# Kernel tuning notes

Hardware: AMD Instinct MI355X
Metric: run time of the kernel (lower is better)

Reference implementation:

```python
import jax, jax.numpy as jnp
import numpy as np
import math

XLEN, YLEN, B = 2048, 1024, 8
XD, YD, HD, YOUT = 1024, 1024, 512, 1024


def setup_inputs() -> dict:
    key = jax.random.key(0)
    ks = jax.random.split(key, 12)

    def lin(kw, kb, out_d, in_d):
        s = 1.0 / math.sqrt(in_d)
        w = jax.random.uniform(kw, (out_d, in_d), jnp.float32, -s, s)
        b = jax.random.uniform(kb, (out_d,), jnp.float32, -s, s)
        return w, b

    Xk_w, Xk_b = lin(ks[0], ks[1], HD, XD)
    Xv_w, Xv_b = lin(ks[2], ks[3], HD, XD)
    Yq_w, Yq_b = lin(ks[4], ks[5], HD, YD)
    Yw_w, Yw_b = lin(ks[6], ks[7], YOUT, YD + HD)

    X = jax.random.normal(ks[8], (XLEN, B, XD), jnp.float32)
    Y = jax.random.normal(ks[9], (YLEN, B, YD), jnp.float32)
    alignment = jax.random.normal(ks[10], (B, YLEN, XLEN), jnp.float32)
    X_pad_mask = jax.random.bernoulli(ks[11], 0.1, (B, YLEN, XLEN))  # True -> mask out
    align_w = jnp.zeros((1,), jnp.float32)  # nn.Parameter([0])

    return {"X": X, "Y": Y, "alignment": alignment, "X_pad_mask": X_pad_mask,
            "Xk_w": Xk_w, "Xk_b": Xk_b, "Xv_w": Xv_w, "Xv_b": Xv_b,
            "Yq_w": Yq_w, "Yq_b": Yq_b, "Yw_w": Yw_w, "Yw_b": Yw_b,
            "align_w": align_w}


def reference(X, Y, alignment, X_pad_mask, Xk_w, Xk_b, Xv_w, Xv_b,
              Yq_w, Yq_b, Yw_w, Yw_b, align_w):
    FMAX = jnp.finfo(X.dtype).max
    # projections (torch Linear: x @ W.T + b)
    xk = X @ Xk_w.T + Xk_b                     # (x, b, hd)
    yq = Y @ Yq_w.T + Yq_b                     # (y, b, hd)
    # scaled cross-attention logits
    logit = jnp.einsum('xbd,ybd->byx', xk, yq) / math.sqrt(xk.shape[-1])
    # gated alignment bias + clamp
    logit = logit + jax.nn.sigmoid(align_w[0]) * alignment
    logit = jnp.maximum(logit, -FMAX)
    # pad-mask additive fill (-FMAX) then clamp (matches masked_fill + add + clamp)
    logit = jnp.maximum(logit + jnp.where(X_pad_mask, -FMAX, 0.0), -FMAX)
    attn = jax.nn.softmax(logit, axis=-1)      # (b, y, x); dropout = identity (eval)
    xv = X @ Xv_w.T + Xv_b                     # (x, b, hd)
    attn_feat = jnp.einsum('byx,xbh->ybh', attn, xv)  # (y, b, hd)
    concat = jnp.concatenate([Y, attn_feat], axis=-1)  # (y, b, yd+hd)
    return concat @ Yw_w.T + Yw_b              # (y, b, y_outdim)
```

## Files before the change

### kernel.cpp

```cpp
#include <hip/hip_runtime.h>


#define FMAXF 3.402823466e38f

typedef __attribute__((ext_vector_type(8))) __bf16 bf16x8;
typedef __attribute__((ext_vector_type(4))) float f32x4;

static __device__ __forceinline__ short f2b(float f) {
  union { float f; unsigned u; } x; x.f = f;
  unsigned r = (x.u + 0x7FFFu + ((x.u >> 16) & 1u)) >> 16;
  return (short)r;
}
static __device__ __forceinline__ float b2f(short s) {
  union { unsigned u; float f; } x; x.u = ((unsigned)(unsigned short)s) << 16;
  return x.f;
}

static __device__ __forceinline__ void gl_lds16(const short* g, short* l) {
  __builtin_amdgcn_global_load_lds(
      (const __attribute__((address_space(1))) void*)g,
      (__attribute__((address_space(3))) void*)l, 16, 0, 0);
}


struct EpiKV {
  static constexpr bool staged = true;
  static constexpr bool expm = false;
  static constexpr bool norm = false;
  short* xk; short* xv; const float* kb; const float* vb;
  __device__ float bias_at(int n) const { return n < 512 ? kb[n] : vb[n - 512]; }
  __device__ void store(int bz, int m, int n, int4 v) const {
    int b = m & 7; long x = m >> 3;
    if (n < 512) *(int4*)(xk + ((long)b * 2048 + x) * 512 + n) = v;
    else         *(int4*)(xv + ((long)b * 2048 + x) * 512 + (n - 512)) = v;
  }
};

struct EpiYq {
  static constexpr bool staged = true;
  static constexpr bool expm = false;
  static constexpr bool norm = false;
  short* out; const float* bias;
  __device__ float bias_at(int n) const { return bias[n]; }
  __device__ void store(int bz, int m, int n, int4 v) const {
    *(int4*)(out + (((long)(m & 7)) * 1024 + (m >> 3)) * 512 + n) = v;
  }
};

struct EpiLogitExp {
  static constexpr bool staged = true;
  static constexpr bool expm = true;
  static constexpr bool norm = false;
  short* out;
  const float* align;
  const int* mask;
  const float* alw;
  float* rowsum;
  __device__ float bias_at(int n) const { return 0.0f; }
  __device__ void store(int bz, int m, int n, int4 v) const {
    *(int4*)(out + ((long)bz * 1024 + m) * 2048 + n) = v;
  }
};

struct EpiConcatNorm {
  static constexpr bool staged = true;
  static constexpr bool expm = false;
  static constexpr bool norm = true;
  short* out; const float* rowsum;
  __device__ float bias_at(int n) const { return 0.0f; }
  __device__ void store(int bz, int m, int n, int4 v) const {
    *(int4*)(out + ((long)m * 8 + bz) * 1536 + 1024 + n) = v;
  }
};

struct EpiOut {
  static constexpr bool staged = false;
  static constexpr bool expm = false;
  static constexpr bool norm = false;
  float* out; const float* bias;
  __device__ void direct(int bz, int m, int n, float v) const {
    out[(long)m * 1024 + n] = v + bias[n];
  }
};

template <int TM, typename Epi>
__global__ __launch_bounds__(256) void gemm_mt(
    const short* __restrict__ A, long sAb, int lda,
    const short* __restrict__ B, long sBb, int ldb,
    int K, int tlog, Epi epi) {
  constexpr int R = TM + 128;
  constexpr int SEGS = R / 32;
  constexpr int LDSN = (R * 64 > TM * 128) ? R * 64 : TM * 128;
  __shared__ short S[LDSN];

  const int tid = threadIdx.x;
  const int lane = tid & 63, wave = tid >> 6;
  const int bz = blockIdx.z;

  const int id = blockIdx.x;
  const int xcd = id & 7;
  const int rr = id >> 3;
  const int n0 = (rr & ((1 << tlog) - 1)) * 128;
  const int m0 = (((rr >> tlog) << 3) + xcd) * TM;

  const short* gp[SEGS];
#pragma unroll
  for (int t = 0; t < SEGS; t++) {
    int slot = t * 256 + tid;
    int row = slot >> 3;
    int gcol = ((slot & 7) ^ (row & 7)) * 8;
    gp[t] = (row < TM)
                ? A + (long)bz * sAb + (long)(m0 + row) * lda + gcol
                : B + (long)bz * sBb + (long)(n0 + row - TM) * ldb + gcol;
  }

  const int wm = (TM == 128) ? (wave & 1) * 64 : 0;
  const int wn = (TM == 128) ? (wave >> 1) * 64 : wave * 32;
  constexpr int MI = 4;
  constexpr int MJ = (TM == 128) ? 4 : 2;
  const int quad = lane >> 4, l16 = lane & 15;
  const int xr = l16 & 7;

  f32x4 acc[MI][MJ] = {};

  for (int k0 = 0; k0 < K; k0 += 64) {
#pragma unroll
    for (int t = 0; t < SEGS; t++)
      gl_lds16(gp[t] + k0, S + (t * 256 + tid) * 8);
    __syncthreads();

#pragma unroll
    for (int kk = 0; kk < 2; kk++) {
      union { int4 v; bf16x8 f; } a[MI], b[MJ];
      const int g = ((kk << 2) + quad);
#pragma unroll
      for (int i = 0; i < MI; i++)
        a[i].v = *(const int4*)(S + (wm + i * 16 + l16) * 64 + (g ^ xr) * 8);
#pragma unroll
      for (int j = 0; j < MJ; j++)
        b[j].v = *(const int4*)(S + (TM + wn + j * 16 + l16) * 64 + (g ^ xr) * 8);
#pragma unroll
      for (int i = 0; i < MI; i++)
#pragma unroll
        for (int j = 0; j < MJ; j++)
          acc[i][j] = __builtin_amdgcn_mfma_f32_16x16x32_bf16(a[i].f, b[j].f,
                                                              acc[i][j], 0, 0, 0);
    }
    __syncthreads();
  }

  if constexpr (Epi::staged) {
    if constexpr (Epi::norm) {
#pragma unroll
      for (int i = 0; i < MI; i++)
#pragma unroll
        for (int r = 0; r < 4; r++) {
          const int row = wm + i * 16 + quad * 4 + r;
          const float inv = 1.0f / epi.rowsum[(long)bz * 1024 + m0 + row];
#pragma unroll
          for (int j = 0; j < MJ; j++)
            S[row * 128 + wn + j * 16 + l16] = f2b(acc[i][j][r] * inv);
        }
    } else {
#pragma unroll
      for (int j = 0; j < MJ; j++) {
        const int c = wn + j * 16 + l16;
        const float bj = epi.bias_at(n0 + c);
#pragma unroll
        for (int i = 0; i < MI; i++)
#pragma unroll
          for (int r = 0; r < 4; r++)
            S[(wm + i * 16 + quad * 4 + r) * 128 + c] = f2b(acc[i][j][r] + bj);
      }
    }
    __syncthreads();

    if constexpr (Epi::expm) {
      const float g = 1.0f / (1.0f + __expf(-epi.alw[0]));
      const float scale = 0.04419417382415922f;
#pragma unroll
      for (int t = 0; t < TM / 16; t++) {
        const int c = t * 256 + tid;
        const int row = c >> 4, colc = (c & 15) * 8;
        const long gy = (long)bz * 1024 + m0 + row;
        const float* ap = epi.align + gy * 2048 + n0 + colc;
        const int*   mp = epi.mask + gy * 2048 + n0 + colc;
        float4 a0 = *(const float4*)ap;
        float4 a1 = *(const float4*)(ap + 4);
        int4 q0 = *(const int4*)mp;
        int4 q1 = *(const int4*)(mp + 4);
        union { short s[8]; int4 v; } d;
        d.v = *(const int4*)(S + row * 128 + colc);
        float e[8];
        e[0] = q0.x ? 0.0f : __expf(fmaf(b2f(d.s[0]), scale, g * a0.x));
        e[1] = q0.y ? 0.0f : __expf(fmaf(b2f(d.s[1]), scale, g * a0.y));
        e[2] = q0.z ? 0.0f : __expf(fmaf(b2f(d.s[2]), scale, g * a0.z));
        e[3] = q0.w ? 0.0f : __expf(fmaf(b2f(d.s[3]), scale, g * a0.w));
        e[4] = q1.x ? 0.0f : __expf(fmaf(b2f(d.s[4]), scale, g * a1.x));
        e[5] = q1.y ? 0.0f : __expf(fmaf(b2f(d.s[5]), scale, g * a1.y));
        e[6] = q1.z ? 0.0f : __expf(fmaf(b2f(d.s[6]), scale, g * a1.z));
        e[7] = q1.w ? 0.0f : __expf(fmaf(b2f(d.s[7]), scale, g * a1.w));
        float part = 0.0f;
#pragma unroll
        for (int k = 0; k < 8; k++) { part += e[k]; d.s[k] = f2b(e[k]); }
        epi.store(bz, m0 + row, n0 + colc, d.v);
        part += __shfl_xor(part, 1);
        part += __shfl_xor(part, 2);
        part += __shfl_xor(part, 4);
        part += __shfl_xor(part, 8);
        if ((tid & 15) == 0) atomicAdd(epi.rowsum + gy, part);
      }
    } else {
#pragma unroll
      for (int t = 0; t < TM / 16; t++) {
        int c = t * 256 + tid;
        int row = c >> 4, colc = (c & 15) * 8;
        int4 v = *(const int4*)(S + row * 128 + colc);
        epi.store(bz, m0 + row, n0 + colc, v);
      }
    }
  } else {
#pragma unroll
    for (int i = 0; i < MI; i++)
#pragma unroll
      for (int j = 0; j < MJ; j++)
#pragma unroll
        for (int r = 0; r < 4; r++)
          epi.direct(bz, m0 + wm + i * 16 + quad * 4 + r,
                     n0 + wn + j * 16 + l16, acc[i][j][r]);
  }
}

__global__ __launch_bounds__(256) void cvt_f32_bf16(const float* __restrict__ in,
                                                    short* __restrict__ out,
                                                    long n4) {
  long i = (long)blockIdx.x * 256 + threadIdx.x;
  if (i >= n4) return;
  float4 f = ((const float4*)in)[i];
  union { short s[4]; long long v; } o;
  o.s[0] = f2b(f.x); o.s[1] = f2b(f.y); o.s[2] = f2b(f.z); o.s[3] = f2b(f.w);
  ((long long*)out)[i] = o.v;
}

__global__ __launch_bounds__(256) void cvt_weights(
    const float* __restrict__ xk_w, const float* __restrict__ xv_w,
    const float* __restrict__ yq_w, const float* __restrict__ yw_w,
    short* __restrict__ wkv, short* __restrict__ wyq, short* __restrict__ wyw,
    float* __restrict__ rowsum) {
  long i = (long)blockIdx.x * 256 + threadIdx.x;
  if (i < 8192) rowsum[i] = 0.0f;
  const float* src; long long* dst; long off;
  if (i < 131072)      { src = xk_w; dst = (long long*)wkv; off = i; }
  else if (i < 262144) { src = xv_w; dst = (long long*)wkv + 131072; off = i - 131072; }
  else if (i < 393216) { src = yq_w; dst = (long long*)wyq; off = i - 262144; }
  else                 { src = yw_w; dst = (long long*)wyw; off = i - 393216; }
  float4 f = ((const float4*)src)[off];
  union { short s[4]; long long v; } o;
  o.s[0] = f2b(f.x); o.s[1] = f2b(f.y); o.s[2] = f2b(f.z); o.s[3] = f2b(f.w);
  dst[off] = o.v;
}

__global__ __launch_bounds__(256) void cvt_y_concat(const float* __restrict__ in,
                                                    short* __restrict__ out) {
  long idx = (long)blockIdx.x * 256 + threadIdx.x;
  long row = idx >> 8;
  int c = (int)(idx & 255) << 2;
  float4 f = *(const float4*)(in + row * 1024 + c);
  union { short s[4]; unsigned long long v; } o;
  o.s[0] = f2b(f.x); o.s[1] = f2b(f.y); o.s[2] = f2b(f.z); o.s[3] = f2b(f.w);
  *(unsigned long long*)(out + row * 1536 + c) = o.v;
}

__global__ __launch_bounds__(256) void transpose_xv(const short* __restrict__ xv,
                                                    short* __restrict__ xvt) {
  __shared__ short t[32][36];
  const int b = blockIdx.z;
  const long x0 = (long)blockIdx.x * 32, h0 = (long)blockIdx.y * 32;
  const int r = threadIdx.x >> 3, c = (threadIdx.x & 7) * 4;
  const short* src = xv + ((long)b * 2048 + x0 + r) * 512 + h0 + c;
  *(int2*)&t[r][c] = *(const int2*)src;
  __syncthreads();
  union { short s[4]; int2 v; } o;
  o.s[0] = t[c + 0][r]; o.s[1] = t[c + 1][r];
  o.s[2] = t[c + 2][r]; o.s[3] = t[c + 3][r];
  short* dst = xvt + ((long)b * 512 + h0 + r) * 2048 + x0 + c;
  *(int2*)dst = o.v;
}


extern "C" void kernel_launch(void* const* d_in, const int* in_sizes, int n_in,
                              void* d_out, int out_size, void* d_ws, size_t ws_size,
                              hipStream_t stream) {
  const float* X    = (const float*)d_in[0];
  const float* Y    = (const float*)d_in[1];
  const float* alig = (const float*)d_in[2];
  const int*   mask = (const int*)d_in[3];
  const float* Xk_w = (const float*)d_in[4];
  const float* Xk_b = (const float*)d_in[5];
  const float* Xv_w = (const float*)d_in[6];
  const float* Xv_b = (const float*)d_in[7];
  const float* Yq_w = (const float*)d_in[8];
  const float* Yq_b = (const float*)d_in[9];
  const float* Yw_w = (const float*)d_in[10];
  const float* Yw_b = (const float*)d_in[11];
  const float* alw  = (const float*)d_in[12];
  float* out = (float*)d_out;

  char* ws = (char*)d_ws;
  short* xbf    = (short*)(ws + 0);
  short* E      = (short*)(ws + 0);
  short* xk     = (short*)(ws + 33554432);
  short* xv     = (short*)(ws + 50331648);
  short* xvt    = (short*)(ws + 67108864);
  short* yq     = (short*)(ws + 83886080);
  short* concat = (short*)(ws + 92274688);
  short* wkv    = (short*)(ws + 117440512);
  short* wyq    = (short*)(ws + 119537664);
  short* wyw    = (short*)(ws + 120586240);
  float* rowsum = (float*)(ws + 123731968);

  cvt_f32_bf16<<<16384, 256, 0, stream>>>(X, xbf, 4194304);
  cvt_y_concat<<<8192, 256, 0, stream>>>(Y, concat);
  cvt_weights<<<3072, 256, 0, stream>>>(Xk_w, Xv_w, Yq_w, Yw_w, wkv, wyq, wyw,
                                        rowsum);

  gemm_mt<128, EpiKV><<<dim3(1024, 1, 1), 256, 0, stream>>>(
      xbf, 0, 1024, wkv, 0, 1024, 1024, 3, EpiKV{xk, xv, Xk_b, Xv_b});

  gemm_mt<64, EpiYq><<<dim3(512, 1, 1), 256, 0, stream>>>(
      concat, 0, 1536, wyq, 0, 1024, 1024, 2, EpiYq{yq, Yq_b});

  transpose_xv<<<dim3(64, 16, 8), 256, 0, stream>>>(xv, xvt);

  gemm_mt<128, EpiLogitExp><<<dim3(128, 1, 8), 256, 0, stream>>>(
      yq, (long)1024 * 512, 512, xk, (long)2048 * 512, 512, 512, 4,
      EpiLogitExp{E, alig, mask, alw, rowsum});

  gemm_mt<64, EpiConcatNorm><<<dim3(64, 1, 8), 256, 0, stream>>>(
      E, (long)1024 * 2048, 2048, xvt, (long)512 * 2048, 2048, 2048, 2,
      EpiConcatNorm{concat, rowsum});

  gemm_mt<128, EpiOut><<<dim3(512, 1, 1), 256, 0, stream>>>(
      concat, 0, 1536, wyw, 0, 1536, 1536, 3, EpiOut{out, Yw_b});
}
```

Before: 423.3 us.

## Add 512-thread double-buffered GEMM with larger tiles for KV, logit and output GEMMs

Introduces a new gemm_p kernel using 512 threads, 256x128 or 128x256 tiles, double-buffered LDS with async global-to-LDS loads prefetched two k-steps ahead, and s_setprio around the MFMA block. Three of the GEMMs (KV projection, logit+exp, output projection) switch to it, and the exp/mask epilogue moves out of the old kernel into the new one, with the staged epilogue done in two halves. The aim is more data reuse per tile and overlap of loads with MFMA. The cost is fewer blocks per launch, which can underfill the CUs, plus higher register pressure.

```diff
diff --git a/kernel.cpp b/kernel.cpp
--- a/kernel.cpp
+++ b/kernel.cpp
@@ -83,6 +83,188 @@
   }
 };
 
+template <int BM, int BN, typename Epi>
+__global__ __launch_bounds__(512, 2) void gemm_p(
+    const short* __restrict__ A, long sAb, int lda,
+    const short* __restrict__ B, long sBb, int ldb,
+    int K, int tlog, Epi epi) {
+  constexpr int RT = BM + BN;
+  constexpr int TS = RT * 32;
+  __shared__ short S[2 * TS];
+
+  const int tid = threadIdx.x;
+  const int lane = tid & 63, wave = tid >> 6;
+  const int quad = lane >> 4, l16 = lane & 15;
+  const int bz = blockIdx.z;
+
+  const int id = blockIdx.x;
+  const int xcd = id & 7;
+  const int rr = id >> 3;
+  const int n0 = (rr & ((1 << tlog) - 1)) * BN;
+  const int m0 = (((rr >> tlog) << 3) + xcd) * BM;
+
+  const short* gp[3];
+#pragma unroll
+  for (int u = 0; u < 3; u++) {
+    int slot = u * 512 + tid;
+    int row = slot >> 2;
+    int g = (slot & 3) ^ ((row ^ (row >> 2)) & 3);
+    gp[u] = (row < BM
+                 ? A + (long)bz * sAb + (long)(m0 + row) * lda
+                 : B + (long)bz * sBb + (long)(n0 + row - BM) * ldb) + g * 8;
+  }
+
+  const int wm = (BM == 256) ? (wave >> 1) * 64 : (wave >> 2) * 64;
+  const int wn = (BM == 256) ? (wave & 1) * 64 : (wave & 3) * 64;
+
+  int aoff[4], boff[4];
+#pragma unroll
+  for (int i = 0; i < 4; i++) {
+    int ra = wm + i * 16 + l16;
+    aoff[i] = ra * 32 + ((quad ^ ((ra ^ (ra >> 2)) & 3)) * 8);
+    int rb = BM + wn + i * 16 + l16;
+    boff[i] = rb * 32 + ((quad ^ ((rb ^ (rb >> 2)) & 3)) * 8);
+  }
+
+  f32x4 acc[4][4] = {};
+  const int nt = K >> 5;
+
+#pragma unroll
+  for (int u = 0; u < 3; u++)
+    gl_lds16(gp[u], S + (u * 512 + tid) * 8);
+#pragma unroll
+  for (int u = 0; u < 3; u++)
+    gl_lds16(gp[u] + 32, S + TS + (u * 512 + tid) * 8);
+
+  for (int t = 0; t < nt; t++) {
+    const short* Sb = S + (t & 1) * TS;
+    if (t + 1 < nt) asm volatile("s_waitcnt vmcnt(3)" ::: "memory");
+    else            asm volatile("s_waitcnt vmcnt(0)" ::: "memory");
+    __builtin_amdgcn_s_barrier();
+    asm volatile("" ::: "memory");
+
+    union { int4 v; bf16x8 f; } a[4], b[4];
+#pragma unroll
+    for (int i = 0; i < 4; i++) a[i].v = *(const int4*)(Sb + aoff[i]);
+#pragma unroll
+    for (int j = 0; j < 4; j++) b[j].v = *(const int4*)(Sb + boff[j]);
+    __builtin_amdgcn_s_setprio(1);
+#pragma unroll
+    for (int i = 0; i < 4; i++)
+#pragma unroll
+      for (int j = 0; j < 4; j++)
+        acc[i][j] = __builtin_amdgcn_mfma_f32_16x16x32_bf16(a[i].f, b[j].f,
+                                                            acc[i][j], 0, 0, 0);
+    __builtin_amdgcn_s_setprio(0);
+
+    asm volatile("s_waitcnt lgkmcnt(0)" ::: "memory");
+    __builtin_amdgcn_s_barrier();
+    asm volatile("" ::: "memory");
+    if (t + 2 < nt) {
+      short* Sw = S + (t & 1) * TS;
+      const int ko = (t + 2) * 32;
+#pragma unroll
+      for (int u = 0; u < 3; u++)
+        gl_lds16(gp[u] + ko, Sw + (u * 512 + tid) * 8);
+    }
+  }
+
+  if constexpr (Epi::staged) {
+    constexpr bool splitM = (BM == 256);
+#pragma unroll
+    for (int h = 0; h < 2; h++) {
+      __syncthreads();
+      if constexpr (splitM) {
+        if ((wm >> 7) == h) {
+          const int lr = wm & 127;
+#pragma unroll
+          for (int j = 0; j < 4; j++) {
+            const int c = wn + j * 16 + l16;
+            const float bj = epi.bias_at(n0 + c);
+#pragma unroll
+            for (int i = 0; i < 4; i++)
+#pragma unroll
+              for (int r = 0; r < 4; r++)
+                S[(lr + i * 16 + quad * 4 + r) * 128 + c] =
+                    f2b(acc[i][j][r] + bj);
+          }
+        }
+      } else {
+        if ((wn >> 7) == h) {
+          const int lc = wn & 127;
+#pragma unroll
+          for (int j = 0; j < 4; j++) {
+            const int cl = lc + j * 16 + l16;
+            const float bj = epi.bias_at(n0 + h * 128 + cl);
+#pragma unroll
+            for (int i = 0; i < 4; i++)
+#pragma unroll
+              for (int r = 0; r < 4; r++)
+                S[(wm + i * 16 + quad * 4 + r) * 128 + cl] =
+                    f2b(acc[i][j][r] + bj);
+          }
+        }
+      }
+      __syncthreads();
+      const int gm0 = splitM ? m0 + h * 128 : m0;
+      const int gn0 = splitM ? n0 : n0 + h * 128;
+      if constexpr (Epi::expm) {
+        const float g = 1.0f / (1.0f + __expf(-epi.alw[0]));
+        const float scale = 0.04419417382415922f;
+#pragma unroll
+        for (int it = 0; it < 4; it++) {
+          const int c = it * 512 + tid;
+          const int row = c >> 4, colc = (c & 15) * 8;
+          const long gy = (long)bz * 1024 + gm0 + row;
+          const float* ap = epi.align + gy * 2048 + gn0 + colc;
+          const int*   mp = epi.mask + gy * 2048 + gn0 + colc;
+          float4 a0 = *(const float4*)ap;
+          float4 a1 = *(const float4*)(ap + 4);
+          int4 q0 = *(const int4*)mp;
+          int4 q1 = *(const int4*)(mp + 4);
+          union { short s[8]; int4 v; } d;
+          d.v = *(const int4*)(S + row * 128 + colc);
+          float e[8];
+          e[0] = q0.x ? 0.0f : __expf(fmaf(b2f(d.s[0]), scale, g * a0.x));
+          e[1] = q0.y ? 0.0f : __expf(fmaf(b2f(d.s[1]), scale, g * a0.y));
+          e[2] = q0.z ? 0.0f : __expf(fmaf(b2f(d.s[2]), scale, g * a0.z));
+          e[3] = q0.w ? 0.0f : __expf(fmaf(b2f(d.s[3]), scale, g * a0.w));
+          e[4] = q1.x ? 0.0f : __expf(fmaf(b2f(d.s[4]), scale, g * a1.x));
+          e[5] = q1.y ? 0.0f : __expf(fmaf(b2f(d.s[5]), scale, g * a1.y));
+          e[6] = q1.z ? 0.0f : __expf(fmaf(b2f(d.s[6]), scale, g * a1.z));
+          e[7] = q1.w ? 0.0f : __expf(fmaf(b2f(d.s[7]), scale, g * a1.w));
+          float part = 0.0f;
+#pragma unroll
+          for (int k = 0; k < 8; k++) { part += e[k]; d.s[k] = f2b(e[k]); }
+          epi.store(bz, gm0 + row, gn0 + colc, d.v);
+          part += __shfl_xor(part, 1);
+          part += __shfl_xor(part, 2);
+          part += __shfl_xor(part, 4);
+          part += __shfl_xor(part, 8);
+          if ((tid & 15) == 0) atomicAdd(epi.rowsum + gy, part);
+        }
+      } else {
+#pragma unroll
+        for (int it = 0; it < 4; it++) {
+          const int c = it * 512 + tid;
+          const int row = c >> 4, colc = (c & 15) * 8;
+          int4 v = *(const int4*)(S + row * 128 + colc);
+          epi.store(bz, gm0 + row, gn0 + colc, v);
+        }
+      }
+    }
+  } else {
+#pragma unroll
+    for (int i = 0; i < 4; i++)
+#pragma unroll
+      for (int j = 0; j < 4; j++)
+#pragma unroll
+        for (int r = 0; r < 4; r++)
+          epi.direct(bz, m0 + wm + i * 16 + quad * 4 + r,
+                     n0 + wn + j * 16 + l16, acc[i][j][r]);
+  }
+}
+
 template <int TM, typename Epi>
 __global__ __launch_bounds__(256) void gemm_mt(
     const short* __restrict__ A, long sAb, int lda,
@@ -174,50 +356,12 @@
       }
     }
     __syncthreads();
-
-    if constexpr (Epi::expm) {
-      const float g = 1.0f / (1.0f + __expf(-epi.alw[0]));
-      const float scale = 0.04419417382415922f;
-#pragma unroll
-      for (int t = 0; t < TM / 16; t++) {
-        const int c = t * 256 + tid;
-        const int row = c >> 4, colc = (c & 15) * 8;
-        const long gy = (long)bz * 1024 + m0 + row;
-        const float* ap = epi.align + gy * 2048 + n0 + colc;
-        const int*   mp = epi.mask + gy * 2048 + n0 + colc;
-        float4 a0 = *(const float4*)ap;
-        float4 a1 = *(const float4*)(ap + 4);
-        int4 q0 = *(const int4*)mp;
-        int4 q1 = *(const int4*)(mp + 4);
-        union { short s[8]; int4 v; } d;
-        d.v = *(const int4*)(S + row * 128 + colc);
-        float e[8];
-        e[0] = q0.x ? 0.0f : __expf(fmaf(b2f(d.s[0]), scale, g * a0.x));
-        e[1] = q0.y ? 0.0f : __expf(fmaf(b2f(d.s[1]), scale, g * a0.y));
-        e[2] = q0.z ? 0.0f : __expf(fmaf(b2f(d.s[2]), scale, g * a0.z));
-        e[3] = q0.w ? 0.0f : __expf(fmaf(b2f(d.s[3]), scale, g * a0.w));
-        e[4] = q1.x ? 0.0f : __expf(fmaf(b2f(d.s[4]), scale, g * a1.x));
-        e[5] = q1.y ? 0.0f : __expf(fmaf(b2f(d.s[5]), scale, g * a1.y));
-        e[6] = q1.z ? 0.0f : __expf(fmaf(b2f(d.s[6]), scale, g * a1.z));
-        e[7] = q1.w ? 0.0f : __expf(fmaf(b2f(d.s[7]), scale, g * a1.w));
-        float part = 0.0f;
-#pragma unroll
-        for (int k = 0; k < 8; k++) { part += e[k]; d.s[k] = f2b(e[k]); }
-        epi.store(bz, m0 + row, n0 + colc, d.v);
-        part += __shfl_xor(part, 1);
-        part += __shfl_xor(part, 2);
-        part += __shfl_xor(part, 4);
-        part += __shfl_xor(part, 8);
-        if ((tid & 15) == 0) atomicAdd(epi.rowsum + gy, part);
-      }
-    } else {
-#pragma unroll
-      for (int t = 0; t < TM / 16; t++) {
-        int c = t * 256 + tid;
-        int row = c >> 4, colc = (c & 15) * 8;
-        int4 v = *(const int4*)(S + row * 128 + colc);
-        epi.store(bz, m0 + row, n0 + colc, v);
-      }
+#pragma unroll
+    for (int t = 0; t < TM / 16; t++) {
+      int c = t * 256 + tid;
+      int row = c >> 4, colc = (c & 15) * 8;
+      int4 v = *(const int4*)(S + row * 128 + colc);
+      epi.store(bz, m0 + row, n0 + colc, v);
     }
   } else {
 #pragma unroll
@@ -324,7 +468,7 @@
   cvt_weights<<<3072, 256, 0, stream>>>(Xk_w, Xv_w, Yq_w, Yw_w, wkv, wyq, wyw,
                                         rowsum);
 
-  gemm_mt<128, EpiKV><<<dim3(1024, 1, 1), 256, 0, stream>>>(
+  gemm_p<256, 128, EpiKV><<<dim3(512, 1, 1), 512, 0, stream>>>(
       xbf, 0, 1024, wkv, 0, 1024, 1024, 3, EpiKV{xk, xv, Xk_b, Xv_b});
 
   gemm_mt<64, EpiYq><<<dim3(512, 1, 1), 256, 0, stream>>>(
@@ -332,14 +476,14 @@
 
   transpose_xv<<<dim3(64, 16, 8), 256, 0, stream>>>(xv, xvt);
 
-  gemm_mt<128, EpiLogitExp><<<dim3(128, 1, 8), 256, 0, stream>>>(
-      yq, (long)1024 * 512, 512, xk, (long)2048 * 512, 512, 512, 4,
+  gemm_p<128, 256, EpiLogitExp><<<dim3(64, 1, 8), 512, 0, stream>>>(
+      yq, (long)1024 * 512, 512, xk, (long)2048 * 512, 512, 512, 3,
       EpiLogitExp{E, alig, mask, alw, rowsum});
 
   gemm_mt<64, EpiConcatNorm><<<dim3(64, 1, 8), 256, 0, stream>>>(
       E, (long)1024 * 2048, 2048, xvt, (long)512 * 2048, 2048, 2048, 2,
       EpiConcatNorm{concat, rowsum});
 
-  gemm_mt<128, EpiOut><<<dim3(512, 1, 1), 256, 0, stream>>>(
+  gemm_p<256, 128, EpiOut><<<dim3(256, 1, 1), 512, 0, stream>>>(
       concat, 0, 1536, wyw, 0, 1536, 1536, 3, EpiOut{out, Yw_b});
 }
```

Result: no change. 424.7 us (+0.3%).

## Fuse xv transpose into KV GEMM epilogue, merge conversions, swizzle LDS staging

Applied to the files above, without the earlier changes.

The KV projection epilogue now writes the V half straight into the transposed xvt layout through LDS, which removes the separate transpose kernel and the intermediate xv buffer. The three conversion kernels are merged into one launch. The staging LDS uses an XOR swizzle to cut bank conflicts. The batched logit and AV GEMMs map batch onto the XCD index instead of blockIdx.z. The transposed epilogue gathers from LDS one short at a time, which adds LDS traffic in exchange for saving a full round trip of xv through global memory.

```diff
diff --git a/kernel.cpp b/kernel.cpp
--- a/kernel.cpp
+++ b/kernel.cpp
@@ -27,12 +27,11 @@
   static constexpr bool staged = true;
   static constexpr bool expm = false;
   static constexpr bool norm = false;
-  short* xk; short* xv; const float* kb; const float* vb;
+  static constexpr bool kvt = true;
+  short* xk; short* xvt; const float* kb; const float* vb;
   __device__ float bias_at(int n) const { return n < 512 ? kb[n] : vb[n - 512]; }
   __device__ void store(int bz, int m, int n, int4 v) const {
-    int b = m & 7; long x = m >> 3;
-    if (n < 512) *(int4*)(xk + ((long)b * 2048 + x) * 512 + n) = v;
-    else         *(int4*)(xv + ((long)b * 2048 + x) * 512 + (n - 512)) = v;
+    *(int4*)(xk + (((long)(m & 7)) * 2048 + (m >> 3)) * 512 + n) = v;
   }
 };
 
@@ -40,6 +39,7 @@
   static constexpr bool staged = true;
   static constexpr bool expm = false;
   static constexpr bool norm = false;
+  static constexpr bool kvt = false;
   short* out; const float* bias;
   __device__ float bias_at(int n) const { return bias[n]; }
   __device__ void store(int bz, int m, int n, int4 v) const {
@@ -51,6 +51,7 @@
   static constexpr bool staged = true;
   static constexpr bool expm = true;
   static constexpr bool norm = false;
+  static constexpr bool kvt = false;
   short* out;
   const float* align;
   const int* mask;
@@ -66,6 +67,7 @@
   static constexpr bool staged = true;
   static constexpr bool expm = false;
   static constexpr bool norm = true;
+  static constexpr bool kvt = false;
   short* out; const float* rowsum;
   __device__ float bias_at(int n) const { return 0.0f; }
   __device__ void store(int bz, int m, int n, int4 v) const {
@@ -77,13 +79,14 @@
   static constexpr bool staged = false;
   static constexpr bool expm = false;
   static constexpr bool norm = false;
+  static constexpr bool kvt = false;
   float* out; const float* bias;
   __device__ void direct(int bz, int m, int n, float v) const {
     out[(long)m * 1024 + n] = v + bias[n];
   }
 };
 
-template <int TM, typename Epi>
+template <int TM, typename Epi, bool BXCD = false>
 __global__ __launch_bounds__(256) void gemm_mt(
     const short* __restrict__ A, long sAb, int lda,
     const short* __restrict__ B, long sBb, int ldb,
@@ -95,13 +98,21 @@
 
   const int tid = threadIdx.x;
   const int lane = tid & 63, wave = tid >> 6;
-  const int bz = blockIdx.z;
 
   const int id = blockIdx.x;
-  const int xcd = id & 7;
-  const int rr = id >> 3;
-  const int n0 = (rr & ((1 << tlog) - 1)) * 128;
-  const int m0 = (((rr >> tlog) << 3) + xcd) * TM;
+  int bz, n0, m0;
+  if constexpr (BXCD) {
+    bz = id & 7;
+    const int rr = id >> 3;
+    n0 = (rr & ((1 << tlog) - 1)) * 128;
+    m0 = (rr >> tlog) * TM;
+  } else {
+    bz = blockIdx.z;
+    const int xcd = id & 7;
+    const int rr = id >> 3;
+    n0 = (rr & ((1 << tlog) - 1)) * 128;
+    m0 = (((rr >> tlog) << 3) + xcd) * TM;
+  }
 
   const short* gp[SEGS];
 #pragma unroll
@@ -150,6 +161,9 @@
   }
 
   if constexpr (Epi::staged) {
+    auto sco = [](int row, int col) {
+      return row * 128 + ((((col >> 3) ^ ((row >> 3) & 7)) << 3) | (col & 7));
+    };
     if constexpr (Epi::norm) {
 #pragma unroll
       for (int i = 0; i < MI; i++)
@@ -159,7 +173,7 @@
           const float inv = 1.0f / epi.rowsum[(long)bz * 1024 + m0 + row];
 #pragma unroll
           for (int j = 0; j < MJ; j++)
-            S[row * 128 + wn + j * 16 + l16] = f2b(acc[i][j][r] * inv);
+            S[sco(row, wn + j * 16 + l16)] = f2b(acc[i][j][r] * inv);
         }
     } else {
 #pragma unroll
@@ -170,7 +184,7 @@
         for (int i = 0; i < MI; i++)
 #pragma unroll
           for (int r = 0; r < 4; r++)
-            S[(wm + i * 16 + quad * 4 + r) * 128 + c] = f2b(acc[i][j][r] + bj);
+            S[sco(wm + i * 16 + quad * 4 + r, c)] = f2b(acc[i][j][r] + bj);
       }
     }
     __syncthreads();
@@ -190,7 +204,7 @@
         int4 q0 = *(const int4*)mp;
         int4 q1 = *(const int4*)(mp + 4);
         union { short s[8]; int4 v; } d;
-        d.v = *(const int4*)(S + row * 128 + colc);
+        d.v = *(const int4*)(S + row * 128 + (((c & 15) ^ ((row >> 3) & 7)) << 3));
         float e[8];
         e[0] = q0.x ? 0.0f : __expf(fmaf(b2f(d.s[0]), scale, g * a0.x));
         e[1] = q0.y ? 0.0f : __expf(fmaf(b2f(d.s[1]), scale, g * a0.y));
@@ -210,13 +224,39 @@
         part += __shfl_xor(part, 8);
         if ((tid & 15) == 0) atomicAdd(epi.rowsum + gy, part);
       }
+    } else if constexpr (Epi::kvt) {
+      if (n0 < 512) {
+#pragma unroll
+        for (int t = 0; t < TM / 16; t++) {
+          int c = t * 256 + tid;
+          int row = c >> 4, cg = c & 15;
+          int4 v = *(const int4*)(S + row * 128 + ((cg ^ ((row >> 3) & 7)) << 3));
+          epi.store(bz, m0 + row, n0 + cg * 8, v);
+        }
+      } else {
+        const int x0 = m0 >> 3;
+#pragma unroll
+        for (int it = 0; it < 4; it++) {
+          int c = it * 256 + tid;
+          int hl = c & 127, b = (c >> 7) & 7;
+          union { short s[16]; int4 v[2]; } o;
+#pragma unroll
+          for (int x = 0; x < 16; x++) {
+            int row = x * 8 + b;
+            o.s[x] = S[row * 128 + (((hl >> 3) ^ (x & 7)) << 3) + (hl & 7)];
+          }
+          short* dst = epi.xvt + ((long)b * 512 + (n0 - 512) + hl) * 2048 + x0;
+          *(int4*)dst = o.v[0];
+          *(int4*)(dst + 8) = o.v[1];
+        }
+      }
     } else {
 #pragma unroll
       for (int t = 0; t < TM / 16; t++) {
         int c = t * 256 + tid;
-        int row = c >> 4, colc = (c & 15) * 8;
-        int4 v = *(const int4*)(S + row * 128 + colc);
-        epi.store(bz, m0 + row, n0 + colc, v);
+        int row = c >> 4, cg = c & 15;
+        int4 v = *(const int4*)(S + row * 128 + ((cg ^ ((row >> 3) & 7)) << 3));
+        epi.store(bz, m0 + row, n0 + cg * 8, v);
       }
     }
   } else {
@@ -231,60 +271,38 @@
   }
 }
 
-__global__ __launch_bounds__(256) void cvt_f32_bf16(const float* __restrict__ in,
-                                                    short* __restrict__ out,
-                                                    long n4) {
-  long i = (long)blockIdx.x * 256 + threadIdx.x;
-  if (i >= n4) return;
-  float4 f = ((const float4*)in)[i];
-  union { short s[4]; long long v; } o;
-  o.s[0] = f2b(f.x); o.s[1] = f2b(f.y); o.s[2] = f2b(f.z); o.s[3] = f2b(f.w);
-  ((long long*)out)[i] = o.v;
-}
-
-__global__ __launch_bounds__(256) void cvt_weights(
+__global__ __launch_bounds__(256) void cvt_all(
+    const float* __restrict__ X, const float* __restrict__ Y,
     const float* __restrict__ xk_w, const float* __restrict__ xv_w,
     const float* __restrict__ yq_w, const float* __restrict__ yw_w,
+    short* __restrict__ xbf, short* __restrict__ concat,
     short* __restrict__ wkv, short* __restrict__ wyq, short* __restrict__ wyw,
     float* __restrict__ rowsum) {
   long i = (long)blockIdx.x * 256 + threadIdx.x;
   if (i < 8192) rowsum[i] = 0.0f;
-  const float* src; long long* dst; long off;
-  if (i < 131072)      { src = xk_w; dst = (long long*)wkv; off = i; }
-  else if (i < 262144) { src = xv_w; dst = (long long*)wkv + 131072; off = i - 131072; }
-  else if (i < 393216) { src = yq_w; dst = (long long*)wyq; off = i - 262144; }
-  else                 { src = yw_w; dst = (long long*)wyw; off = i - 393216; }
-  float4 f = ((const float4*)src)[off];
+  float4 f;
+  long long* dst;
+  if (i < 4194304) {
+    f = ((const float4*)X)[i];
+    dst = (long long*)xbf + i;
+  } else if (i < 6291456) {
+    long idx = i - 4194304;
+    long row = idx >> 8;
+    int c = (int)(idx & 255) << 2;
+    f = *(const float4*)(Y + row * 1024 + c);
+    dst = (long long*)(concat + row * 1536 + c);
+  } else {
+    long j = i - 6291456;
+    const float* src; long off;
+    if (j < 131072)      { src = xk_w; dst = (long long*)wkv + j; off = j; }
+    else if (j < 262144) { src = xv_w; dst = (long long*)wkv + j; off = j - 131072; }
+    else if (j < 393216) { src = yq_w; dst = (long long*)wyq + (j - 262144); off = j - 262144; }
+    else                 { src = yw_w; dst = (long long*)wyw + (j - 393216); off = j - 393216; }
+    f = ((const float4*)src)[off];
+  }
   union { short s[4]; long long v; } o;
   o.s[0] = f2b(f.x); o.s[1] = f2b(f.y); o.s[2] = f2b(f.z); o.s[3] = f2b(f.w);
-  dst[off] = o.v;
-}
-
-__global__ __launch_bounds__(256) void cvt_y_concat(const float* __restrict__ in,
-                                                    short* __restrict__ out) {
-  long idx = (long)blockIdx.x * 256 + threadIdx.x;
-  long row = idx >> 8;
-  int c = (int)(idx & 255) << 2;
-  float4 f = *(const float4*)(in + row * 1024 + c);
-  union { short s[4]; unsigned long long v; } o;
-  o.s[0] = f2b(f.x); o.s[1] = f2b(f.y); o.s[2] = f2b(f.z); o.s[3] = f2b(f.w);
-  *(unsigned long long*)(out + row * 1536 + c) = o.v;
-}
-
-__global__ __launch_bounds__(256) void transpose_xv(const short* __restrict__ xv,
-                                                    short* __restrict__ xvt) {
-  __shared__ short t[32][36];
-  const int b = blockIdx.z;
-  const long x0 = (long)blockIdx.x * 32, h0 = (long)blockIdx.y * 32;
-  const int r = threadIdx.x >> 3, c = (threadIdx.x & 7) * 4;
-  const short* src = xv + ((long)b * 2048 + x0 + r) * 512 + h0 + c;
-  *(int2*)&t[r][c] = *(const int2*)src;
-  __syncthreads();
-  union { short s[4]; int2 v; } o;
-  o.s[0] = t[c + 0][r]; o.s[1] = t[c + 1][r];
-  o.s[2] = t[c + 2][r]; o.s[3] = t[c + 3][r];
-  short* dst = xvt + ((long)b * 512 + h0 + r) * 2048 + x0 + c;
-  *(int2*)dst = o.v;
+  *dst = o.v;
 }
 
 
@@ -310,7 +328,6 @@
   short* xbf    = (short*)(ws + 0);
   short* E      = (short*)(ws + 0);
   short* xk     = (short*)(ws + 33554432);
-  short* xv     = (short*)(ws + 50331648);
   short* xvt    = (short*)(ws + 67108864);
   short* yq     = (short*)(ws + 83886080);
   short* concat = (short*)(ws + 92274688);
@@ -319,24 +336,20 @@
   short* wyw    = (short*)(ws + 120586240);
   float* rowsum = (float*)(ws + 123731968);
 
-  cvt_f32_bf16<<<16384, 256, 0, stream>>>(X, xbf, 4194304);
-  cvt_y_concat<<<8192, 256, 0, stream>>>(Y, concat);
-  cvt_weights<<<3072, 256, 0, stream>>>(Xk_w, Xv_w, Yq_w, Yw_w, wkv, wyq, wyw,
-                                        rowsum);
+  cvt_all<<<27648, 256, 0, stream>>>(X, Y, Xk_w, Xv_w, Yq_w, Yw_w,
+                                     xbf, concat, wkv, wyq, wyw, rowsum);
 
   gemm_mt<128, EpiKV><<<dim3(1024, 1, 1), 256, 0, stream>>>(
-      xbf, 0, 1024, wkv, 0, 1024, 1024, 3, EpiKV{xk, xv, Xk_b, Xv_b});
+      xbf, 0, 1024, wkv, 0, 1024, 1024, 3, EpiKV{xk, xvt, Xk_b, Xv_b});
 
   gemm_mt<64, EpiYq><<<dim3(512, 1, 1), 256, 0, stream>>>(
       concat, 0, 1536, wyq, 0, 1024, 1024, 2, EpiYq{yq, Yq_b});
 
-  transpose_xv<<<dim3(64, 16, 8), 256, 0, stream>>>(xv, xvt);
-
-  gemm_mt<128, EpiLogitExp><<<dim3(128, 1, 8), 256, 0, stream>>>(
+  gemm_mt<128, EpiLogitExp, true><<<dim3(1024, 1, 1), 256, 0, stream>>>(
       yq, (long)1024 * 512, 512, xk, (long)2048 * 512, 512, 512, 4,
       EpiLogitExp{E, alig, mask, alw, rowsum});
 
-  gemm_mt<64, EpiConcatNorm><<<dim3(64, 1, 8), 256, 0, stream>>>(
+  gemm_mt<64, EpiConcatNorm, true><<<dim3(512, 1, 1), 256, 0, stream>>>(
       E, (long)1024 * 2048, 2048, xvt, (long)512 * 2048, 2048, 2048, 2,
       EpiConcatNorm{concat, rowsum});
 
```

Measured after the change: 415.7 us. Within noise of the previous version (-1.8%).
